# Performance work log

Hardware: AMD Instinct MI355X
Metric: run time of the kernel (lower is better)

## Reference

```python
import jax, jax.numpy as jnp
import numpy as np

BATCH, N_NODES = 256, 128
NF = MF = 128
EF = AEF = 5


def setup_inputs() -> dict:
    key = jax.random.key(0)
    k = jax.random.split(key, 6)
    afm = jax.random.normal(k[0], (BATCH, N_NODES, NF), dtype=jnp.float32)
    bfm = jax.random.randint(k[1], (BATCH, N_NODES, N_NODES), 0, EF + 1, dtype=jnp.int32)
    a_bfm = jax.random.randint(k[2], (BATCH, N_NODES), 0, AEF + 1, dtype=jnp.int32)
    adj = jax.random.uniform(k[3], (BATCH, N_NODES, N_NODES), dtype=jnp.float32)
    # xavier_uniform for adj_w (ef, mf, nf): fan_in=nf, fan_out=mf per torch convention on last two dims
    lim_w = float(np.sqrt(6.0 / (MF + NF)))
    adj_w = jax.random.uniform(k[4], (EF, MF, NF), minval=-lim_w, maxval=lim_w, dtype=jnp.float32)
    lim_a = float(np.sqrt(6.0 / (AEF + MF)))
    adj_a = jax.random.uniform(k[5], (AEF, MF), minval=-lim_a, maxval=lim_a, dtype=jnp.float32)
    return {"afm": afm, "bfm": bfm, "a_bfm": a_bfm, "adj": adj, "adj_w": adj_w, "adj_a": adj_a}


def reference(afm, bfm, a_bfm, adj, adj_w, adj_a):
    # afm is accepted by the original forward but never used.
    E = adj_w.shape[0] + 1  # zeros row for "no edge" at index 0
    mf, nf = adj_w.shape[1], adj_w.shape[2]
    W_ext = jnp.concatenate([jnp.zeros((1, mf, nf), adj_w.dtype), adj_w], axis=0)  # (E, mf, nf)
    A_ext = jnp.concatenate([jnp.zeros((1, mf), adj_a.dtype), adj_a], axis=0)      # (E_a, mf)
    att = A_ext[a_bfm]  # (b, n, mf); nf == mf required by original matmul
    # Original: msg[b,i,j,m] = sum_k W_ext[bfm[b,i,j], m, k] * att[b, j, k], then sum over i.
    # Contract first per edge type (small), then count-weight instead of gathering huge tensor.
    contrib = jnp.einsum('emn,bjn->bjem', W_ext, att)                  # (b, n, E, mf)
    cnt = jax.nn.one_hot(bfm, E, dtype=contrib.dtype).sum(axis=1)      # (b, j, E) = #{i : bfm[b,i,j]=e}
    messages = jnp.einsum('bje,bjem->bjm', cnt, contrib)               # (b, n, mf)
    return jnp.matmul(adj, messages)                                   # (b, n, mf)
```

## Files before the change

### kernel.cpp

```cpp
#include <hip/hip_runtime.h>

typedef short s16x8 __attribute__((ext_vector_type(8)));
typedef float f32x4 __attribute__((ext_vector_type(4)));

__device__ __forceinline__ short f2bf(float f) {
  union { float f; unsigned u; } cv;
  cv.f = f;
  unsigned u = cv.u;
  u = (u + 0x7FFFu + ((u >> 16) & 1u)) >> 16;
  return (short)u;
}
__device__ __forceinline__ unsigned pk2(float lo, float hi) {
  union { float f; unsigned u; } a, b;
  a.f = lo;
  b.f = hi;
  return (a.u >> 16) | (b.u & 0xFFFF0000u);
}

__global__ __launch_bounds__(256, 4) void hist_mc_kernel(
    const int* __restrict__ bfm, const float* __restrict__ adj_w,
    const float* __restrict__ adj_a, uint2* __restrict__ cnt_g,
    unsigned short* __restrict__ Mc_bf) {
  __shared__ unsigned red[4][8][4][2];
  __shared__ float As[5][128];
  const int t = threadIdx.x;

  if (blockIdx.x >= 1024) {
    const int bi = blockIdx.x - 1024;
    const int e = bi >> 2, mg = bi & 3;
    for (int idx = t; idx < 640; idx += 256) As[idx >> 7][idx & 127] = adj_a[idx];
    __syncthreads();
    const int m = mg * 32 + (t >> 3), ns = t & 7;
    const float* W = adj_w + (size_t)e * 16384 + (size_t)m * 128 + ns * 16;
    float acc[5] = {0.f, 0.f, 0.f, 0.f, 0.f};
#pragma unroll
    for (int it = 0; it < 4; ++it) {
      const float4 wv = *(const float4*)(W + it * 4);
      const float wa[4] = {wv.x, wv.y, wv.z, wv.w};
#pragma unroll
      for (int q = 0; q < 4; ++q) {
        const int n = ns * 16 + it * 4 + q;
#pragma unroll
        for (int a = 0; a < 5; ++a) acc[a] = fmaf(wa[q], As[a][n], acc[a]);
      }
    }
#pragma unroll
    for (int d = 1; d < 8; d <<= 1)
#pragma unroll
      for (int a = 0; a < 5; ++a) acc[a] += __shfl_xor(acc[a], d);
    if (ns == 0)
#pragma unroll
      for (int a = 0; a < 5; ++a)
        Mc_bf[(e * 5 + a) * 128 + m] = (unsigned short)f2bf(acc[a]);
    return;
  }

  const int b = blockIdx.x >> 2, jg = blockIdx.x & 3;
  const int w = t >> 6, l = t & 63, c4 = l & 7, rr = l >> 3;
  const int4* bp = (const int4*)bfm + (size_t)b * 4096 + jg * 8 + c4;
  unsigned pA[4] = {0, 0, 0, 0}, pB[4] = {0, 0, 0, 0};
#pragma unroll
  for (int it = 0; it < 4; ++it) {
    const int i = it * 32 + w * 8 + rr;
    const int4 v = bp[(size_t)i * 32];
    const int vv[4] = {v.x, v.y, v.z, v.w};
#pragma unroll
    for (int jj = 0; jj < 4; ++jj) {
      pA[jj] += (unsigned)(vv[jj] == 1) + ((unsigned)(vv[jj] == 2) << 8) +
                ((unsigned)(vv[jj] == 3) << 16) + ((unsigned)(vv[jj] == 4) << 24);
      pB[jj] += (unsigned)(vv[jj] == 5);
    }
  }
#pragma unroll
  for (int d = 8; d < 64; d <<= 1)
#pragma unroll
    for (int jj = 0; jj < 4; ++jj) {
      pA[jj] += (unsigned)__shfl_xor((int)pA[jj], d);
      pB[jj] += (unsigned)__shfl_xor((int)pB[jj], d);
    }
  if (rr == 0)
#pragma unroll
    for (int jj = 0; jj < 4; ++jj) {
      red[w][c4][jj][0] = pA[jj];
      red[w][c4][jj][1] = pB[jj];
    }
  __syncthreads();
  if (t < 32) {
    unsigned A = 0, B = 0;
    const int cc = t >> 2, jj = t & 3;
#pragma unroll
    for (int w2 = 0; w2 < 4; ++w2) {
      A += red[w2][cc][jj][0];
      B += red[w2][cc][jj][1];
    }
    cnt_g[b * 128 + jg * 32 + t] = make_uint2(A, B);
  }
}

__global__ __launch_bounds__(256, 3) void fused_gemm_kernel(
    const float* __restrict__ adj, const int* __restrict__ a_bfm,
    const uint2* __restrict__ cnt_g, const unsigned short* __restrict__ Mc_bf,
    float* __restrict__ out) {
  __shared__ __align__(16) unsigned short msgsT[128 * 128];
  __shared__ __align__(16) unsigned short P[128 * 40];
  __shared__ __align__(16) unsigned short Mtab[32 * 136];
  const int b = blockIdx.x >> 1, h = blockIdx.x & 1, r0 = h * 64;
  const int t = threadIdx.x;
  const int w = t >> 6, l = t & 63, g = l >> 4, c = l & 15;

  const float* arow = adj + (size_t)b * 16384 + (size_t)(r0 + w * 16 + c) * 128;
  float4 a0[4], a1[4];
#pragma unroll
  for (int kk = 0; kk < 4; ++kk) {
    a0[kk] = *(const float4*)(arow + (kk * 4 + g) * 8);
    a1[kk] = *(const float4*)(arow + (kk * 4 + g) * 8 + 4);
  }

  unsigned cA = 0, cB = 0;
  int av = 0;
  if (t < 128) {
    const uint2 cc2 = cnt_g[b * 128 + t];
    cA = cc2.x;
    cB = cc2.y;
    av = a_bfm[b * 128 + t];
  }
  for (int idx = t; idx < 400; idx += 256) {
    const int row = idx >> 4, c8 = idx & 15;
    *(s16x8*)&Mtab[row * 136 + c8 * 8] = *(const s16x8*)&Mc_bf[row * 128 + c8 * 8];
  }
  for (int idx = t; idx < 7 * 136; idx += 256) Mtab[25 * 136 + idx] = 0;
  for (int idx = t; idx < 640; idx += 256)
    ((uint4*)P)[idx] = make_uint4(0u, 0u, 0u, 0u);
  __syncthreads();

  if (t < 128 && av > 0) {
    const int ai = av - 1;
    unsigned short* Pr = &P[t * 40];
    Pr[ai] = (unsigned short)f2bf((float)(cA & 255u));
    Pr[5 + ai] = (unsigned short)f2bf((float)((cA >> 8) & 255u));
    Pr[10 + ai] = (unsigned short)f2bf((float)((cA >> 16) & 255u));
    Pr[15 + ai] = (unsigned short)f2bf((float)(cA >> 24));
    Pr[20 + ai] = (unsigned short)f2bf((float)(cB & 255u));
  }
  __syncthreads();

  {
    const int m0 = w * 32;
    s16x8 bfr[2];
#pragma unroll
    for (int ct = 0; ct < 2; ++ct)
#pragma unroll
      for (int e = 0; e < 8; ++e)
        bfr[ct][e] = (short)Mtab[(g * 8 + e) * 136 + m0 + ct * 16 + c];
#pragma unroll
    for (int jt = 0; jt < 8; ++jt) {
      const s16x8 afr = *(const s16x8*)&P[(jt * 16 + c) * 40 + g * 8];
#pragma unroll
      for (int ct = 0; ct < 2; ++ct) {
        f32x4 acc = {0.f, 0.f, 0.f, 0.f};
        acc = __builtin_amdgcn_mfma_f32_16x16x32_bf16(afr, bfr[ct], acc, 0, 0, 0);
        const int m = m0 + ct * 16 + c;
        unsigned short* dst =
            &msgsT[m * 128 + (((jt * 2 + (g >> 1)) ^ (m & 15)) << 3) + (g & 1) * 4];
#pragma unroll
        for (int q = 0; q < 4; ++q) dst[q] = (unsigned short)f2bf(acc[q]);
      }
    }
  }

  s16x8 apk[4];
#pragma unroll
  for (int kk = 0; kk < 4; ++kk) {
    unsigned* pu = (unsigned*)&apk[kk];
    pu[0] = pk2(a0[kk].x, a0[kk].y);
    pu[1] = pk2(a0[kk].z, a0[kk].w);
    pu[2] = pk2(a1[kk].x, a1[kk].y);
    pu[3] = pk2(a1[kk].z, a1[kk].w);
  }
  __syncthreads();

  f32x4 acc2[8];
#pragma unroll
  for (int mt = 0; mt < 8; ++mt) acc2[mt] = (f32x4){0.f, 0.f, 0.f, 0.f};
#pragma unroll
  for (int kk = 0; kk < 4; ++kk) {
#pragma unroll
    for (int mt = 0; mt < 8; ++mt) {
      const int m = mt * 16 + c;
      const s16x8 bfr2 =
          *(const s16x8*)&msgsT[m * 128 + (((kk * 4 + g) ^ (m & 15)) << 3)];
      acc2[mt] = __builtin_amdgcn_mfma_f32_16x16x32_bf16(apk[kk], bfr2, acc2[mt], 0, 0, 0);
    }
  }
  float* ob = out + (size_t)b * 16384 + (size_t)(r0 + w * 16) * 128;
#pragma unroll
  for (int mt = 0; mt < 8; ++mt)
#pragma unroll
    for (int q = 0; q < 4; ++q)
      ob[(g * 4 + q) * 128 + mt * 16 + c] = acc2[mt][q];
}

extern "C" void kernel_launch(void* const* d_in, const int* in_sizes, int n_in,
                              void* d_out, int out_size, void* d_ws,
                              size_t ws_size, hipStream_t stream) {
  const int* bfm = (const int*)d_in[1];
  const int* a_bfm = (const int*)d_in[2];
  const float* adj = (const float*)d_in[3];
  const float* adj_w = (const float*)d_in[4];
  const float* adj_a = (const float*)d_in[5];
  float* out = (float*)d_out;

  unsigned short* Mc_bf = (unsigned short*)d_ws;
  uint2* cnt_g = (uint2*)((char*)d_ws + 8192);

  hist_mc_kernel<<<dim3(1044), dim3(256), 0, stream>>>(bfm, adj_w, adj_a,
                                                       cnt_g, Mc_bf);
  fused_gemm_kernel<<<dim3(512), dim3(256), 0, stream>>>(adj, a_bfm, cnt_g,
                                                         Mc_bf, out);
}
```

Measured before the change: 19.54 us.

## Fuse bfm histogram into GEMM kernel and split out Mc precompute

Moves the per-column edge-type counting of bfm into the main GEMM kernel, removing the global count buffer and its write/read round trip. The small Mc table computation becomes its own tiny kernel. Each of the two blocks per batch now reads the whole bfm slab, duplicating that read traffic, and occupancy hint drops to 2 blocks per CU with heavier register use.

```diff
diff --git a/kernel.cpp b/kernel.cpp
--- a/kernel.cpp
+++ b/kernel.cpp
@@ -17,53 +17,78 @@
   return (a.u >> 16) | (b.u & 0xFFFF0000u);
 }
 
-__global__ __launch_bounds__(256, 4) void hist_mc_kernel(
-    const int* __restrict__ bfm, const float* __restrict__ adj_w,
-    const float* __restrict__ adj_a, uint2* __restrict__ cnt_g,
+__global__ __launch_bounds__(256) void precomp_Mc(
+    const float* __restrict__ adj_w, const float* __restrict__ adj_a,
     unsigned short* __restrict__ Mc_bf) {
-  __shared__ unsigned red[4][8][4][2];
   __shared__ float As[5][128];
   const int t = threadIdx.x;
-
-  if (blockIdx.x >= 1024) {
-    const int bi = blockIdx.x - 1024;
-    const int e = bi >> 2, mg = bi & 3;
-    for (int idx = t; idx < 640; idx += 256) As[idx >> 7][idx & 127] = adj_a[idx];
-    __syncthreads();
-    const int m = mg * 32 + (t >> 3), ns = t & 7;
-    const float* W = adj_w + (size_t)e * 16384 + (size_t)m * 128 + ns * 16;
-    float acc[5] = {0.f, 0.f, 0.f, 0.f, 0.f};
-#pragma unroll
-    for (int it = 0; it < 4; ++it) {
-      const float4 wv = *(const float4*)(W + it * 4);
-      const float wa[4] = {wv.x, wv.y, wv.z, wv.w};
-#pragma unroll
-      for (int q = 0; q < 4; ++q) {
-        const int n = ns * 16 + it * 4 + q;
-#pragma unroll
-        for (int a = 0; a < 5; ++a) acc[a] = fmaf(wa[q], As[a][n], acc[a]);
-      }
-    }
-#pragma unroll
-    for (int d = 1; d < 8; d <<= 1)
-#pragma unroll
-      for (int a = 0; a < 5; ++a) acc[a] += __shfl_xor(acc[a], d);
-    if (ns == 0)
-#pragma unroll
-      for (int a = 0; a < 5; ++a)
-        Mc_bf[(e * 5 + a) * 128 + m] = (unsigned short)f2bf(acc[a]);
-    return;
-  }
-
-  const int b = blockIdx.x >> 2, jg = blockIdx.x & 3;
-  const int w = t >> 6, l = t & 63, c4 = l & 7, rr = l >> 3;
-  const int4* bp = (const int4*)bfm + (size_t)b * 4096 + jg * 8 + c4;
+  const int e = blockIdx.x >> 2, mg = blockIdx.x & 3;
+  for (int idx = t; idx < 640; idx += 256) As[idx >> 7][idx & 127] = adj_a[idx];
+  __syncthreads();
+  const int m = mg * 32 + (t >> 3), ns = t & 7;
+  const float* W = adj_w + (size_t)e * 16384 + (size_t)m * 128 + ns * 16;
+  float acc[5] = {0.f, 0.f, 0.f, 0.f, 0.f};
+#pragma unroll
+  for (int it = 0; it < 4; ++it) {
+    const float4 wv = *(const float4*)(W + it * 4);
+    const float wa[4] = {wv.x, wv.y, wv.z, wv.w};
+#pragma unroll
+    for (int q = 0; q < 4; ++q) {
+      const int n = ns * 16 + it * 4 + q;
+#pragma unroll
+      for (int a = 0; a < 5; ++a) acc[a] = fmaf(wa[q], As[a][n], acc[a]);
+    }
+  }
+#pragma unroll
+  for (int d = 1; d < 8; d <<= 1)
+#pragma unroll
+    for (int a = 0; a < 5; ++a) acc[a] += __shfl_xor(acc[a], d);
+  if (ns == 0)
+#pragma unroll
+    for (int a = 0; a < 5; ++a)
+      Mc_bf[(e * 5 + a) * 128 + m] = (unsigned short)f2bf(acc[a]);
+}
+
+__global__ __launch_bounds__(256, 2) void fused_kernel(
+    const int* __restrict__ bfm, const float* __restrict__ adj,
+    const int* __restrict__ a_bfm, const unsigned short* __restrict__ Mc_bf,
+    float* __restrict__ out) {
+  __shared__ __align__(16) unsigned short msgsT[128 * 128];
+  __shared__ __align__(16) unsigned short P[128 * 40];
+  __shared__ __align__(16) unsigned short Mtab[32 * 136];
+  __shared__ unsigned red[4][32][4][2];
+  const int b = blockIdx.x >> 1, h = blockIdx.x & 1, r0 = h * 64;
+  const int t = threadIdx.x, w = t >> 6, l = t & 63, g = l >> 4, c = l & 15;
+
+  const int col4 = t & 31, rr = t >> 5;
+  const int4* bp = (const int4*)bfm + (size_t)b * 4096 + col4;
+  int4 bv[16];
+#pragma unroll
+  for (int it = 0; it < 8; ++it) bv[it] = bp[(size_t)(rr * 16 + it) * 32];
+  s16x8 mst0 = *(const s16x8*)&Mc_bf[t * 8];
+  const bool hasM1 = t < 144;
+  s16x8 mst1 = {0, 0, 0, 0, 0, 0, 0, 0};
+  if (hasM1) mst1 = *(const s16x8*)&Mc_bf[(256 + t) * 8];
+  int av = 0;
+  if (t < 128) av = a_bfm[b * 128 + t];
+#pragma unroll
+  for (int it = 8; it < 16; ++it) bv[it] = bp[(size_t)(rr * 16 + it) * 32];
+  const float* arow = adj + (size_t)b * 16384 + (size_t)(r0 + w * 16 + c) * 128;
+  float4 a0[4], a1[4];
+#pragma unroll
+  for (int kk = 0; kk < 4; ++kk) {
+    a0[kk] = *(const float4*)(arow + (kk * 4 + g) * 8);
+    a1[kk] = *(const float4*)(arow + (kk * 4 + g) * 8 + 4);
+  }
+
+  for (int idx = t; idx < 640; idx += 256)
+    ((uint4*)P)[idx] = make_uint4(0u, 0u, 0u, 0u);
+  for (int idx = t; idx < 7 * 136; idx += 256) Mtab[25 * 136 + idx] = 0;
+
   unsigned pA[4] = {0, 0, 0, 0}, pB[4] = {0, 0, 0, 0};
 #pragma unroll
-  for (int it = 0; it < 4; ++it) {
-    const int i = it * 32 + w * 8 + rr;
-    const int4 v = bp[(size_t)i * 32];
-    const int vv[4] = {v.x, v.y, v.z, v.w};
+  for (int it = 0; it < 16; ++it) {
+    const int vv[4] = {bv[it].x, bv[it].y, bv[it].z, bv[it].w};
 #pragma unroll
     for (int jj = 0; jj < 4; ++jj) {
       pA[jj] += (unsigned)(vv[jj] == 1) + ((unsigned)(vv[jj] == 2) << 8) +
@@ -72,75 +97,39 @@
     }
   }
 #pragma unroll
-  for (int d = 8; d < 64; d <<= 1)
+  for (int jj = 0; jj < 4; ++jj) {
+    pA[jj] += (unsigned)__shfl_xor((int)pA[jj], 32);
+    pB[jj] += (unsigned)__shfl_xor((int)pB[jj], 32);
+  }
+  if (l < 32) {
 #pragma unroll
     for (int jj = 0; jj < 4; ++jj) {
-      pA[jj] += (unsigned)__shfl_xor((int)pA[jj], d);
-      pB[jj] += (unsigned)__shfl_xor((int)pB[jj], d);
-    }
-  if (rr == 0)
-#pragma unroll
-    for (int jj = 0; jj < 4; ++jj) {
-      red[w][c4][jj][0] = pA[jj];
-      red[w][c4][jj][1] = pB[jj];
-    }
-  __syncthreads();
-  if (t < 32) {
+      red[w][l][jj][0] = pA[jj];
+      red[w][l][jj][1] = pB[jj];
+    }
+  }
+  *(s16x8*)&Mtab[(t >> 4) * 136 + (t & 15) * 8] = mst0;
+  if (hasM1) {
+    const int ch = 256 + t;
+    *(s16x8*)&Mtab[(ch >> 4) * 136 + (ch & 15) * 8] = mst1;
+  }
+  __syncthreads();
+
+  if (t < 128 && av > 0) {
     unsigned A = 0, B = 0;
-    const int cc = t >> 2, jj = t & 3;
+    const int c4i = t >> 2, jj = t & 3;
 #pragma unroll
     for (int w2 = 0; w2 < 4; ++w2) {
-      A += red[w2][cc][jj][0];
-      B += red[w2][cc][jj][1];
-    }
-    cnt_g[b * 128 + jg * 32 + t] = make_uint2(A, B);
-  }
-}
-
-__global__ __launch_bounds__(256, 3) void fused_gemm_kernel(
-    const float* __restrict__ adj, const int* __restrict__ a_bfm,
-    const uint2* __restrict__ cnt_g, const unsigned short* __restrict__ Mc_bf,
-    float* __restrict__ out) {
-  __shared__ __align__(16) unsigned short msgsT[128 * 128];
-  __shared__ __align__(16) unsigned short P[128 * 40];
-  __shared__ __align__(16) unsigned short Mtab[32 * 136];
-  const int b = blockIdx.x >> 1, h = blockIdx.x & 1, r0 = h * 64;
-  const int t = threadIdx.x;
-  const int w = t >> 6, l = t & 63, g = l >> 4, c = l & 15;
-
-  const float* arow = adj + (size_t)b * 16384 + (size_t)(r0 + w * 16 + c) * 128;
-  float4 a0[4], a1[4];
-#pragma unroll
-  for (int kk = 0; kk < 4; ++kk) {
-    a0[kk] = *(const float4*)(arow + (kk * 4 + g) * 8);
-    a1[kk] = *(const float4*)(arow + (kk * 4 + g) * 8 + 4);
-  }
-
-  unsigned cA = 0, cB = 0;
-  int av = 0;
-  if (t < 128) {
-    const uint2 cc2 = cnt_g[b * 128 + t];
-    cA = cc2.x;
-    cB = cc2.y;
-    av = a_bfm[b * 128 + t];
-  }
-  for (int idx = t; idx < 400; idx += 256) {
-    const int row = idx >> 4, c8 = idx & 15;
-    *(s16x8*)&Mtab[row * 136 + c8 * 8] = *(const s16x8*)&Mc_bf[row * 128 + c8 * 8];
-  }
-  for (int idx = t; idx < 7 * 136; idx += 256) Mtab[25 * 136 + idx] = 0;
-  for (int idx = t; idx < 640; idx += 256)
-    ((uint4*)P)[idx] = make_uint4(0u, 0u, 0u, 0u);
-  __syncthreads();
-
-  if (t < 128 && av > 0) {
+      A += red[w2][c4i][jj][0];
+      B += red[w2][c4i][jj][1];
+    }
     const int ai = av - 1;
     unsigned short* Pr = &P[t * 40];
-    Pr[ai] = (unsigned short)f2bf((float)(cA & 255u));
-    Pr[5 + ai] = (unsigned short)f2bf((float)((cA >> 8) & 255u));
-    Pr[10 + ai] = (unsigned short)f2bf((float)((cA >> 16) & 255u));
-    Pr[15 + ai] = (unsigned short)f2bf((float)(cA >> 24));
-    Pr[20 + ai] = (unsigned short)f2bf((float)(cB & 255u));
+    Pr[ai] = (unsigned short)f2bf((float)(A & 255u));
+    Pr[5 + ai] = (unsigned short)f2bf((float)((A >> 8) & 255u));
+    Pr[10 + ai] = (unsigned short)f2bf((float)((A >> 16) & 255u));
+    Pr[15 + ai] = (unsigned short)f2bf((float)(A >> 24));
+    Pr[20 + ai] = (unsigned short)f2bf((float)(B & 255u));
   }
   __syncthreads();
 
@@ -189,7 +178,8 @@
       const int m = mt * 16 + c;
       const s16x8 bfr2 =
           *(const s16x8*)&msgsT[m * 128 + (((kk * 4 + g) ^ (m & 15)) << 3)];
-      acc2[mt] = __builtin_amdgcn_mfma_f32_16x16x32_bf16(apk[kk], bfr2, acc2[mt], 0, 0, 0);
+      acc2[mt] =
+          __builtin_amdgcn_mfma_f32_16x16x32_bf16(apk[kk], bfr2, acc2[mt], 0, 0, 0);
     }
   }
   float* ob = out + (size_t)b * 16384 + (size_t)(r0 + w * 16) * 128;
@@ -211,10 +201,8 @@
   float* out = (float*)d_out;
 
   unsigned short* Mc_bf = (unsigned short*)d_ws;
-  uint2* cnt_g = (uint2*)((char*)d_ws + 8192);
-
-  hist_mc_kernel<<<dim3(1044), dim3(256), 0, stream>>>(bfm, adj_w, adj_a,
-                                                       cnt_g, Mc_bf);
-  fused_gemm_kernel<<<dim3(512), dim3(256), 0, stream>>>(adj, a_bfm, cnt_g,
-                                                         Mc_bf, out);
-}
+
+  precomp_Mc<<<dim3(20), dim3(256), 0, stream>>>(adj_w, adj_a, Mc_bf);
+  fused_kernel<<<dim3(512), dim3(256), 0, stream>>>(bfm, adj, a_bfm, Mc_bf,
+                                                    out);
+}
```

Result: slower. 24.60 us (+25.9%).

## Reassociate adj·(P·M) as (adj·P)·M to avoid materializing messages

Applied to the files above, without the earlier changes.

Before, the second kernel built the full 128x128 messages matrix (P·Mc) in LDS and then multiplied adj by it. Now it computes adj·P first, a skinny 128x32 product over the 25 count/attention columns, and then multiplies that by the transposed 32x128 Mc table. This removes the large msgsT LDS buffer and most of the MFMA work. The change also stores Mc transposed with zero padding, switches to 128-thread blocks over quarter row tiles (1024 blocks), and replaces __syncthreads with a raw barrier. The intermediate adj·P is rounded to bf16, which adds a different rounding point.

```diff
diff --git a/kernel.cpp b/kernel.cpp
--- a/kernel.cpp
+++ b/kernel.cpp
@@ -20,7 +20,7 @@
 __global__ __launch_bounds__(256, 4) void hist_mc_kernel(
     const int* __restrict__ bfm, const float* __restrict__ adj_w,
     const float* __restrict__ adj_a, uint2* __restrict__ cnt_g,
-    unsigned short* __restrict__ Mc_bf) {
+    unsigned short* __restrict__ McT) {
   __shared__ unsigned red[4][8][4][2];
   __shared__ float As[5][128];
   const int t = threadIdx.x;
@@ -48,10 +48,14 @@
     for (int d = 1; d < 8; d <<= 1)
 #pragma unroll
       for (int a = 0; a < 5; ++a) acc[a] += __shfl_xor(acc[a], d);
-    if (ns == 0)
+    if (ns == 0) {
 #pragma unroll
       for (int a = 0; a < 5; ++a)
-        Mc_bf[(e * 5 + a) * 128 + m] = (unsigned short)f2bf(acc[a]);
+        McT[m * 40 + e * 5 + a] = (unsigned short)f2bf(acc[a]);
+      if (e == 0)
+#pragma unroll
+        for (int r = 25; r < 40; ++r) McT[m * 40 + r] = 0;
+    }
     return;
   }
 
@@ -97,77 +101,62 @@
   }
 }
 
-__global__ __launch_bounds__(256, 3) void fused_gemm_kernel(
+__global__ __launch_bounds__(128, 3) void skinny_kernel(
     const float* __restrict__ adj, const int* __restrict__ a_bfm,
-    const uint2* __restrict__ cnt_g, const unsigned short* __restrict__ Mc_bf,
+    const uint2* __restrict__ cnt_g, const unsigned short* __restrict__ McT,
     float* __restrict__ out) {
-  __shared__ __align__(16) unsigned short msgsT[128 * 128];
-  __shared__ __align__(16) unsigned short P[128 * 40];
-  __shared__ __align__(16) unsigned short Mtab[32 * 136];
-  const int b = blockIdx.x >> 1, h = blockIdx.x & 1, r0 = h * 64;
-  const int t = threadIdx.x;
-  const int w = t >> 6, l = t & 63, g = l >> 4, c = l & 15;
-
-  const float* arow = adj + (size_t)b * 16384 + (size_t)(r0 + w * 16 + c) * 128;
+  __shared__ __align__(16) unsigned short Pt[32 * 128];
+  __shared__ __align__(16) unsigned short Mt[128 * 40];
+  __shared__ __align__(16) unsigned short Qs[2 * 16 * 40];
+  const int bq = blockIdx.x, b = bq >> 2, qq = bq & 3;
+  const int t = threadIdx.x, w = t >> 6, l = t & 63, g = l >> 4, c = l & 15;
+  const int row0 = qq * 32 + w * 16;
+
+  const uint2 cc2 = cnt_g[b * 128 + t];
+  const int av = a_bfm[b * 128 + t];
+  s16x8 mst[5];
+#pragma unroll
+  for (int i = 0; i < 5; ++i) mst[i] = *(const s16x8*)&McT[(i * 128 + t) * 8];
+  const float* arow = adj + (size_t)b * 16384 + (size_t)(row0 + c) * 128;
   float4 a0[4], a1[4];
 #pragma unroll
   for (int kk = 0; kk < 4; ++kk) {
-    a0[kk] = *(const float4*)(arow + (kk * 4 + g) * 8);
-    a1[kk] = *(const float4*)(arow + (kk * 4 + g) * 8 + 4);
-  }
-
-  unsigned cA = 0, cB = 0;
-  int av = 0;
-  if (t < 128) {
-    const uint2 cc2 = cnt_g[b * 128 + t];
-    cA = cc2.x;
-    cB = cc2.y;
-    av = a_bfm[b * 128 + t];
-  }
-  for (int idx = t; idx < 400; idx += 256) {
-    const int row = idx >> 4, c8 = idx & 15;
-    *(s16x8*)&Mtab[row * 136 + c8 * 8] = *(const s16x8*)&Mc_bf[row * 128 + c8 * 8];
-  }
-  for (int idx = t; idx < 7 * 136; idx += 256) Mtab[25 * 136 + idx] = 0;
-  for (int idx = t; idx < 640; idx += 256)
-    ((uint4*)P)[idx] = make_uint4(0u, 0u, 0u, 0u);
-  __syncthreads();
-
-  if (t < 128 && av > 0) {
+    a0[kk] = *(const float4*)(arow + kk * 32 + g * 8);
+    a1[kk] = *(const float4*)(arow + kk * 32 + g * 8 + 4);
+  }
+
+#pragma unroll
+  for (int i = 0; i < 4; ++i)
+    ((uint4*)Pt)[i * 128 + t] = make_uint4(0u, 0u, 0u, 0u);
+#pragma unroll
+  for (int i = 0; i < 5; ++i) *(s16x8*)&Mt[(i * 128 + t) * 8] = mst[i];
+  asm volatile("s_waitcnt lgkmcnt(0)" ::: "memory");
+  __builtin_amdgcn_s_barrier();
+
+  if (av > 0) {
     const int ai = av - 1;
-    unsigned short* Pr = &P[t * 40];
-    Pr[ai] = (unsigned short)f2bf((float)(cA & 255u));
-    Pr[5 + ai] = (unsigned short)f2bf((float)((cA >> 8) & 255u));
-    Pr[10 + ai] = (unsigned short)f2bf((float)((cA >> 16) & 255u));
-    Pr[15 + ai] = (unsigned short)f2bf((float)(cA >> 24));
-    Pr[20 + ai] = (unsigned short)f2bf((float)(cB & 255u));
-  }
-  __syncthreads();
-
-  {
-    const int m0 = w * 32;
-    s16x8 bfr[2];
-#pragma unroll
-    for (int ct = 0; ct < 2; ++ct)
-#pragma unroll
-      for (int e = 0; e < 8; ++e)
-        bfr[ct][e] = (short)Mtab[(g * 8 + e) * 136 + m0 + ct * 16 + c];
-#pragma unroll
-    for (int jt = 0; jt < 8; ++jt) {
-      const s16x8 afr = *(const s16x8*)&P[(jt * 16 + c) * 40 + g * 8];
-#pragma unroll
-      for (int ct = 0; ct < 2; ++ct) {
-        f32x4 acc = {0.f, 0.f, 0.f, 0.f};
-        acc = __builtin_amdgcn_mfma_f32_16x16x32_bf16(afr, bfr[ct], acc, 0, 0, 0);
-        const int m = m0 + ct * 16 + c;
-        unsigned short* dst =
-            &msgsT[m * 128 + (((jt * 2 + (g >> 1)) ^ (m & 15)) << 3) + (g & 1) * 4];
-#pragma unroll
-        for (int q = 0; q < 4; ++q) dst[q] = (unsigned short)f2bf(acc[q]);
-      }
-    }
-  }
-
+    const int chunk = t >> 3, off = t & 7;
+    const float cf[5] = {(float)(cc2.x & 255u), (float)((cc2.x >> 8) & 255u),
+                         (float)((cc2.x >> 16) & 255u), (float)(cc2.x >> 24),
+                         (float)(cc2.y & 255u)};
+#pragma unroll
+    for (int ei = 0; ei < 5; ++ei) {
+      const int r = ei * 5 + ai;
+      Pt[r * 128 + ((chunk ^ (r & 15)) << 3) + off] =
+          (unsigned short)f2bf(cf[ei]);
+    }
+  }
+  asm volatile("s_waitcnt lgkmcnt(0)" ::: "memory");
+  __builtin_amdgcn_s_barrier();
+
+  s16x8 bP[4][2];
+#pragma unroll
+  for (int kk = 0; kk < 4; ++kk)
+#pragma unroll
+    for (int ct = 0; ct < 2; ++ct) {
+      const int r = ct * 16 + c;
+      bP[kk][ct] = *(const s16x8*)&Pt[r * 128 + (((kk * 4 + g) ^ (r & 15)) << 3)];
+    }
   s16x8 apk[4];
 #pragma unroll
   for (int kk = 0; kk < 4; ++kk) {
@@ -177,27 +166,32 @@
     pu[2] = pk2(a1[kk].x, a1[kk].y);
     pu[3] = pk2(a1[kk].z, a1[kk].w);
   }
-  __syncthreads();
-
-  f32x4 acc2[8];
-#pragma unroll
-  for (int mt = 0; mt < 8; ++mt) acc2[mt] = (f32x4){0.f, 0.f, 0.f, 0.f};
-#pragma unroll
-  for (int kk = 0; kk < 4; ++kk) {
-#pragma unroll
-    for (int mt = 0; mt < 8; ++mt) {
-      const int m = mt * 16 + c;
-      const s16x8 bfr2 =
-          *(const s16x8*)&msgsT[m * 128 + (((kk * 4 + g) ^ (m & 15)) << 3)];
-      acc2[mt] = __builtin_amdgcn_mfma_f32_16x16x32_bf16(apk[kk], bfr2, acc2[mt], 0, 0, 0);
-    }
-  }
-  float* ob = out + (size_t)b * 16384 + (size_t)(r0 + w * 16) * 128;
-#pragma unroll
-  for (int mt = 0; mt < 8; ++mt)
+  f32x4 accQ[2] = {{0.f, 0.f, 0.f, 0.f}, {0.f, 0.f, 0.f, 0.f}};
+#pragma unroll
+  for (int kk = 0; kk < 4; ++kk)
+#pragma unroll
+    for (int ct = 0; ct < 2; ++ct)
+      accQ[ct] =
+          __builtin_amdgcn_mfma_f32_16x16x32_bf16(apk[kk], bP[kk][ct], accQ[ct], 0, 0, 0);
+
+  unsigned short* qsw = &Qs[w * 16 * 40];
+#pragma unroll
+  for (int ct = 0; ct < 2; ++ct)
 #pragma unroll
     for (int q = 0; q < 4; ++q)
-      ob[(g * 4 + q) * 128 + mt * 16 + c] = acc2[mt][q];
+      qsw[(g * 4 + q) * 40 + ct * 16 + c] = (unsigned short)f2bf(accQ[ct][q]);
+  const s16x8 aQ = *(const s16x8*)&qsw[c * 40 + g * 8];
+
+  float* ob = out + (size_t)b * 16384 + (size_t)row0 * 128;
+#pragma unroll
+  for (int mt = 0; mt < 8; ++mt) {
+    const s16x8 bM = *(const s16x8*)&Mt[(mt * 16 + c) * 40 + g * 8];
+    f32x4 acc2 = {0.f, 0.f, 0.f, 0.f};
+    acc2 = __builtin_amdgcn_mfma_f32_16x16x32_bf16(aQ, bM, acc2, 0, 0, 0);
+#pragma unroll
+    for (int q = 0; q < 4; ++q)
+      ob[(g * 4 + q) * 128 + mt * 16 + c] = acc2[q];
+  }
 }
 
 extern "C" void kernel_launch(void* const* d_in, const int* in_sizes, int n_in,
@@ -210,11 +204,11 @@
   const float* adj_a = (const float*)d_in[5];
   float* out = (float*)d_out;
 
-  unsigned short* Mc_bf = (unsigned short*)d_ws;
-  uint2* cnt_g = (uint2*)((char*)d_ws + 8192);
+  unsigned short* McT = (unsigned short*)d_ws;
+  uint2* cnt_g = (uint2*)((char*)d_ws + 16384);
 
   hist_mc_kernel<<<dim3(1044), dim3(256), 0, stream>>>(bfm, adj_w, adj_a,
-                                                       cnt_g, Mc_bf);
-  fused_gemm_kernel<<<dim3(512), dim3(256), 0, stream>>>(adj, a_bfm, cnt_g,
-                                                         Mc_bf, out);
-}
+                                                       cnt_g, McT);
+  skinny_kernel<<<dim3(1024), dim3(128), 0, stream>>>(adj, a_bfm, cnt_g, McT,
+                                                      out);
+}
```

Result: faster. 17.86 us (-8.6%).
